# Performance work log

Measured on AMD Instinct MI355X. Metric: run time of the kernel, lower is better.

Reference implementation:

```python
import jax, jax.numpy as jnp
import numpy as np

B, D, H = 2048, 32, 512  # batch, state dim (x has D+1 cols incl. logdet slot), MLP hidden


def setup_inputs() -> dict:
    key = jax.random.key(0)
    ks = jax.random.split(key, 6)
    return {
        "t": jax.random.uniform(ks[0], (1,), dtype=jnp.float32),
        "x": jax.random.normal(ks[1], (B, D + 1), dtype=jnp.float32),
        "W1": jax.random.normal(ks[2], (D + 1, H), dtype=jnp.float32) / np.float32(np.sqrt(D + 1)),
        "b1": jnp.zeros((H,), jnp.float32),
        "W2": jax.random.normal(ks[3], (H, H), dtype=jnp.float32) / np.float32(np.sqrt(H)),
        "b2": jnp.zeros((H,), jnp.float32),
        "W3": jax.random.normal(ks[4], (H, D), dtype=jnp.float32) / np.float32(np.sqrt(H)),
        "b3": jnp.zeros((D,), jnp.float32),
    }


def _vf_single(xi, t, W1, b1, W2, b2, W3, b3):
    # single-sample vector field: R^D -> R^D, time t concatenated as a feature
    inp = jnp.concatenate([xi, t])  # (D+1,)
    h = jnp.tanh(inp @ W1 + b1)
    h = jnp.tanh(h @ W2 + b2)
    return h @ W3 + b3


def reference(t, x, W1, b1, W2, b2, W3, b3):
    xs = x[..., :-1]  # (B, D): drop logdet accumulator column
    # batched vector field dx = vf(t, xs)
    tt = jnp.broadcast_to(t, (xs.shape[0], 1))
    inp = jnp.concatenate([xs, tt], axis=-1)  # (B, D+1)
    h = jnp.tanh(inp @ W1 + b1)
    h = jnp.tanh(h @ W2 + b2)
    dx = h @ W3 + b3  # (B, D)
    # exact divergence: trace of per-sample Jacobian (torch vmap(jacrev) equivalent)
    f = lambda xi: _vf_single(xi, t, W1, b1, W2, b2, W3, b3)
    div = jax.vmap(lambda xi: jnp.trace(jax.jacfwd(f)(xi)))(xs)  # (B,)
    return jnp.concatenate([dx, div[:, None]], axis=-1)  # (B, D+1)
```

## Files before the change

### kernel.cpp

```cpp
#include <hip/hip_runtime.h>
#include <math.h>

constexpr int NB = 2048;
constexpr int ND = 32;
constexpr int NH = 512;
constexpr int NKI = NH / 32;

typedef __bf16 bf16x8 __attribute__((ext_vector_type(8)));
typedef __bf16 bf16x4 __attribute__((ext_vector_type(4)));
typedef float floatx4 __attribute__((ext_vector_type(4)));

__device__ inline float fast_tanh(float x) {
  float e = __expf(2.f * x);
  return 1.f - 2.f / (e + 1.f);
}


__global__ __launch_bounds__(256) void k_pre(
    const float* __restrict__ W1, const float* __restrict__ W2,
    const float* __restrict__ W3, __bf16* __restrict__ W2p,
    __bf16* __restrict__ Mp, float* __restrict__ W3T,
    float* __restrict__ out) {
  int g = blockIdx.x * 256 + threadIdx.x;
  for (int idx = g; idx < NB * (ND + 1); idx += 65536) out[idx] = 0.f;
  if (g < ND * NH)
    W3T[g] = W3[(g & (NH - 1)) * ND + (g >> 9)];

  bool doM = blockIdx.x >= 128;
  int gid = (blockIdx.x & 127) * 256 + threadIdx.x;
  int lane = gid & 63;
  int ki = (gid >> 6) & (NKI - 1);
  int ct = gid >> 10;
  int n = ct * 16 + (lane & 15);
  int k0 = ki * 32 + (lane >> 4) * 8;
  long off = (long)gid * 8;

  if (!doM) {
    __bf16 v[8];
#pragma unroll
    for (int j = 0; j < 8; ++j) v[j] = (__bf16)W2[(k0 + j) * NH + n];
    *(bf16x8*)(W2p + off) = *(bf16x8*)v;
  } else {
    float acc[8];
#pragma unroll
    for (int j = 0; j < 8; ++j) acc[j] = 0.f;
    for (int i = 0; i < ND; ++i) {
      float w3 = W3[n * ND + i];
      float4 u = *(const float4*)&W1[i * NH + k0];
      float4 v = *(const float4*)&W1[i * NH + k0 + 4];
      acc[0] += w3 * u.x; acc[1] += w3 * u.y;
      acc[2] += w3 * u.z; acc[3] += w3 * u.w;
      acc[4] += w3 * v.x; acc[5] += w3 * v.y;
      acc[6] += w3 * v.z; acc[7] += w3 * v.w;
    }
    __bf16 v[8];
#pragma unroll
    for (int j = 0; j < 8; ++j)
      v[j] = (__bf16)(W2[(k0 + j) * NH + n] * acc[j]);
    *(bf16x8*)(Mp + off) = *(bf16x8*)v;
  }
}

__global__ __launch_bounds__(256) void k_main(
    const float* __restrict__ x, const float* __restrict__ t,
    const float* __restrict__ W1, const float* __restrict__ b1,
    const __bf16* __restrict__ W2p, const __bf16* __restrict__ Mp,
    const float* __restrict__ b2, const float* __restrict__ W3T,
    const float* __restrict__ b3, float* __restrict__ out) {
  __shared__ __bf16 aH[16 * NH];
  __shared__ __bf16 aD[16 * NH];
  __shared__ float xs[16][36];
  __shared__ float h2s[16][260];
  __shared__ float divred[4][16];

  int bid = blockIdx.x;
  int rt = bid >> 1;
  int half = bid & 1;
  int tid = threadIdx.x;

  for (int idx = tid; idx < 16 * 33; idx += 256) {
    int r = idx / 33, i = idx - r * 33;
    xs[r][i] = x[(rt * 16 + r) * (ND + 1) + i];
  }
  float tv = t[0];
  __syncthreads();

  {
    int r = tid >> 4;
    int cb = (tid & 15) * 4;
#pragma unroll
    for (int it = 0; it < 8; ++it) {
      int c0 = cb + it * 64;
      float4 bb = *(const float4*)&b1[c0];
      float a0 = bb.x, a1 = bb.y, a2 = bb.z, a3 = bb.w;
#pragma unroll
      for (int i = 0; i < ND; ++i) {
        float xv = xs[r][i];
        float4 w = *(const float4*)&W1[i * NH + c0];
        a0 += xv * w.x; a1 += xv * w.y; a2 += xv * w.z; a3 += xv * w.w;
      }
      {
        float4 w = *(const float4*)&W1[ND * NH + c0];
        a0 += tv * w.x; a1 += tv * w.y; a2 += tv * w.z; a3 += tv * w.w;
      }
      float h0 = fast_tanh(a0), h1 = fast_tanh(a1);
      float h2 = fast_tanh(a2), h3 = fast_tanh(a3);
      __bf16 hv[4] = {(__bf16)h0, (__bf16)h1, (__bf16)h2, (__bf16)h3};
      __bf16 dv[4] = {(__bf16)(1.f - h0 * h0), (__bf16)(1.f - h1 * h1),
                      (__bf16)(1.f - h2 * h2), (__bf16)(1.f - h3 * h3)};
      int ki = c0 >> 5;
      int lane = r | (((c0 >> 3) & 3) << 4);
      int j = c0 & 7;
      int ofs = (ki * 64 + lane) * 8 + j;
      *(bf16x4*)(aH + ofs) = *(bf16x4*)hv;
      *(bf16x4*)(aD + ofs) = *(bf16x4*)dv;
    }
  }
  __syncthreads();

  int w = tid >> 6, lane = tid & 63;
  int col = lane & 15, quad = lane >> 4;
  int ct0 = half * 16 + w * 4;

  floatx4 accH[4] = {{0,0,0,0},{0,0,0,0},{0,0,0,0},{0,0,0,0}};
  floatx4 accM[4] = {{0,0,0,0},{0,0,0,0},{0,0,0,0},{0,0,0,0}};
#pragma unroll 2
  for (int ki = 0; ki < NKI; ++ki) {
    bf16x8 ah = *(const bf16x8*)(aH + (ki * 64 + lane) * 8);
    bf16x8 ad = *(const bf16x8*)(aD + (ki * 64 + lane) * 8);
#pragma unroll
    for (int c = 0; c < 4; ++c) {
      long boff = ((long)((ct0 + c) * NKI + ki) * 64 + lane) * 8;
      bf16x8 bw = *(const bf16x8*)(W2p + boff);
      bf16x8 bm = *(const bf16x8*)(Mp + boff);
      accH[c] = __builtin_amdgcn_mfma_f32_16x16x32_bf16(ah, bw, accH[c], 0, 0, 0);
      accM[c] = __builtin_amdgcn_mfma_f32_16x16x32_bf16(ad, bm, accM[c], 0, 0, 0);
    }
  }

  float divv[4] = {0.f, 0.f, 0.f, 0.f};
#pragma unroll
  for (int c = 0; c < 4; ++c) {
    int n = (ct0 + c) * 16 + col;
    int nc = (w * 4 + c) * 16 + col;
    float bb = b2[n];
#pragma unroll
    for (int r = 0; r < 4; ++r) {
      float h2 = fast_tanh(accH[c][r] + bb);
      h2s[quad * 4 + r][nc] = h2;
      divv[r] += accM[c][r] * (1.f - h2 * h2);
    }
  }
#pragma unroll
  for (int r = 0; r < 4; ++r) {
    float v = divv[r];
    v += __shfl_xor(v, 1);
    v += __shfl_xor(v, 2);
    v += __shfl_xor(v, 4);
    v += __shfl_xor(v, 8);
    if (col == 0) divred[w][quad * 4 + r] = v;
  }
  __syncthreads();
  if (tid < 16) {
    float v = divred[0][tid] + divred[1][tid] + divred[2][tid] + divred[3][tid];
    atomicAdd(&out[(rt * 16 + tid) * (ND + 1) + ND], v);
  }

  int row = tid & 15;
  int i0 = tid >> 4;
  const float* w3a = W3T + (long)(i0 * 2 + 0) * NH + half * 256;
  const float* w3b = W3T + (long)(i0 * 2 + 1) * NH + half * 256;
  float a0 = 0.f, a1 = 0.f;
#pragma unroll 4
  for (int kk = 0; kk < 256; kk += 4) {
    float4 h = *(const float4*)&h2s[row][kk];
    float4 wa = *(const float4*)&w3a[kk];
    float4 wb = *(const float4*)&w3b[kk];
    a0 += h.x * wa.x + h.y * wa.y + h.z * wa.z + h.w * wa.w;
    a1 += h.x * wb.x + h.y * wb.y + h.z * wb.z + h.w * wb.w;
  }
  if (half == 0) { a0 += b3[i0 * 2]; a1 += b3[i0 * 2 + 1]; }
  float* orow = out + (long)(rt * 16 + row) * (ND + 1);
  atomicAdd(&orow[i0 * 2], a0);
  atomicAdd(&orow[i0 * 2 + 1], a1);
}

extern "C" void kernel_launch(void* const* d_in, const int* in_sizes, int n_in,
                              void* d_out, int out_size, void* d_ws, size_t ws_size,
                              hipStream_t stream) {
  const float* t  = (const float*)d_in[0];
  const float* x  = (const float*)d_in[1];
  const float* W1 = (const float*)d_in[2];
  const float* b1 = (const float*)d_in[3];
  const float* W2 = (const float*)d_in[4];
  const float* b2 = (const float*)d_in[5];
  const float* W3 = (const float*)d_in[6];
  const float* b3 = (const float*)d_in[7];
  float* out = (float*)d_out;

  __bf16* W2p = (__bf16*)d_ws;
  __bf16* Mp  = W2p + NH * NH;
  float*  W3T = (float*)(Mp + NH * NH);

  k_pre<<<256, 256, 0, stream>>>(W1, W2, W3, W2p, Mp, W3T, out);
  k_main<<<256, 256, 0, stream>>>(x, t, W1, b1, W2p, Mp, b2, W3T, b3, out);
}
```

Before: 104.7 us.

## Compute first layer with MFMA and retile main kernel to 32 rows by quarter columns

Moves the first-layer matmul (x concatenated with t, times W1) from scalar FMAs onto bf16 MFMA, using a packed W1 prepared in the pre-kernel. The main kernel now handles 32 rows by a quarter of the hidden columns per block instead of 16 rows by a half, so each W2/M fragment is reused across two row tiles. This is meant to cut redundant first-layer work and global weight traffic per output. The cost is that each block recomputes the full first layer for its 32 rows across four column-quarter blocks, and W1 and x are now rounded to bf16.

```diff
diff --git a/kernel.cpp b/kernel.cpp
--- a/kernel.cpp
+++ b/kernel.cpp
@@ -7,7 +7,6 @@
 constexpr int NKI = NH / 32;
 
 typedef __bf16 bf16x8 __attribute__((ext_vector_type(8)));
-typedef __bf16 bf16x4 __attribute__((ext_vector_type(4)));
 typedef float floatx4 __attribute__((ext_vector_type(4)));
 
 __device__ inline float fast_tanh(float x) {
@@ -20,11 +19,25 @@
     const float* __restrict__ W1, const float* __restrict__ W2,
     const float* __restrict__ W3, __bf16* __restrict__ W2p,
     __bf16* __restrict__ Mp, float* __restrict__ W3T,
-    float* __restrict__ out) {
+    __bf16* __restrict__ W1p, float* __restrict__ out) {
   int g = blockIdx.x * 256 + threadIdx.x;
   for (int idx = g; idx < NB * (ND + 1); idx += 65536) out[idx] = 0.f;
   if (g < ND * NH)
     W3T[g] = W3[(g & (NH - 1)) * ND + (g >> 9)];
+  if (g < 4096) {
+    int lane1 = g & 63;
+    int ki1 = (g >> 6) & 1;
+    int ct1 = g >> 7;
+    int n1 = ct1 * 16 + (lane1 & 15);
+    int k0 = ki1 * 32 + (lane1 >> 4) * 8;
+    __bf16 v[8];
+#pragma unroll
+    for (int j = 0; j < 8; ++j) {
+      int k = k0 + j;
+      v[j] = (k <= ND) ? (__bf16)W1[k * NH + n1] : (__bf16)0.f;
+    }
+    *(bf16x8*)(W1p + (long)g * 8) = *(bf16x8*)v;
+  }
 
   bool doM = blockIdx.x >= 128;
   int gid = (blockIdx.x & 127) * 256 + threadIdx.x;
@@ -63,126 +76,150 @@
 
 __global__ __launch_bounds__(256) void k_main(
     const float* __restrict__ x, const float* __restrict__ t,
-    const float* __restrict__ W1, const float* __restrict__ b1,
+    const __bf16* __restrict__ W1p, const float* __restrict__ b1,
     const __bf16* __restrict__ W2p, const __bf16* __restrict__ Mp,
     const float* __restrict__ b2, const float* __restrict__ W3T,
     const float* __restrict__ b3, float* __restrict__ out) {
-  __shared__ __bf16 aH[16 * NH];
-  __shared__ __bf16 aD[16 * NH];
-  __shared__ float xs[16][36];
-  __shared__ float h2s[16][260];
-  __shared__ float divred[4][16];
+  __shared__ __bf16 xf[2 * 2 * 64 * 8];
+  __shared__ __bf16 aH[2 * 16 * 64 * 8];
+  __shared__ __bf16 aD[2 * 16 * 64 * 8];
+  __shared__ float h2s[32][132];
+  __shared__ float divred[4][32];
 
   int bid = blockIdx.x;
-  int rt = bid >> 1;
-  int half = bid & 1;
+  int rb = bid >> 2;
+  int q = bid & 3;
   int tid = threadIdx.x;
-
-  for (int idx = tid; idx < 16 * 33; idx += 256) {
-    int r = idx / 33, i = idx - r * 33;
-    xs[r][i] = x[(rt * 16 + r) * (ND + 1) + i];
-  }
-  float tv = t[0];
-  __syncthreads();
-
-  {
-    int r = tid >> 4;
-    int cb = (tid & 15) * 4;
-#pragma unroll
-    for (int it = 0; it < 8; ++it) {
-      int c0 = cb + it * 64;
-      float4 bb = *(const float4*)&b1[c0];
-      float a0 = bb.x, a1 = bb.y, a2 = bb.z, a3 = bb.w;
-#pragma unroll
-      for (int i = 0; i < ND; ++i) {
-        float xv = xs[r][i];
-        float4 w = *(const float4*)&W1[i * NH + c0];
-        a0 += xv * w.x; a1 += xv * w.y; a2 += xv * w.z; a3 += xv * w.w;
-      }
-      {
-        float4 w = *(const float4*)&W1[ND * NH + c0];
-        a0 += tv * w.x; a1 += tv * w.y; a2 += tv * w.z; a3 += tv * w.w;
-      }
-      float h0 = fast_tanh(a0), h1 = fast_tanh(a1);
-      float h2 = fast_tanh(a2), h3 = fast_tanh(a3);
-      __bf16 hv[4] = {(__bf16)h0, (__bf16)h1, (__bf16)h2, (__bf16)h3};
-      __bf16 dv[4] = {(__bf16)(1.f - h0 * h0), (__bf16)(1.f - h1 * h1),
-                      (__bf16)(1.f - h2 * h2), (__bf16)(1.f - h3 * h3)};
-      int ki = c0 >> 5;
-      int lane = r | (((c0 >> 3) & 3) << 4);
-      int j = c0 & 7;
-      int ofs = (ki * 64 + lane) * 8 + j;
-      *(bf16x4*)(aH + ofs) = *(bf16x4*)hv;
-      *(bf16x4*)(aD + ofs) = *(bf16x4*)dv;
-    }
-  }
-  __syncthreads();
-
   int w = tid >> 6, lane = tid & 63;
   int col = lane & 15, quad = lane >> 4;
-  int ct0 = half * 16 + w * 4;
-
-  floatx4 accH[4] = {{0,0,0,0},{0,0,0,0},{0,0,0,0},{0,0,0,0}};
-  floatx4 accM[4] = {{0,0,0,0},{0,0,0,0},{0,0,0,0},{0,0,0,0}};
+  float tv = t[0];
+
+  {
+    int lane0 = tid & 63;
+    int ki0 = (tid >> 6) & 1;
+    int rt0 = tid >> 7;
+    int row = rb * 32 + rt0 * 16 + (lane0 & 15);
+    int k0 = ki0 * 32 + (lane0 >> 4) * 8;
+    __bf16 v[8];
+#pragma unroll
+    for (int j = 0; j < 8; ++j) {
+      int k = k0 + j;
+      float val = (k < ND) ? x[(long)row * (ND + 1) + k] : (k == ND ? tv : 0.f);
+      v[j] = (__bf16)val;
+    }
+    *(bf16x8*)(xf + (long)tid * 8) = *(bf16x8*)v;
+  }
+  __syncthreads();
+
+  {
+    bf16x8 xa[2][2];
+#pragma unroll
+    for (int rt = 0; rt < 2; ++rt)
+#pragma unroll
+      for (int ki = 0; ki < 2; ++ki)
+        xa[rt][ki] = *(const bf16x8*)(xf + ((rt * 2 + ki) * 64 + lane) * 8);
+#pragma unroll 2
+    for (int c8 = 0; c8 < 8; ++c8) {
+      int ct1 = w * 8 + c8;
+      floatx4 ac0 = {0, 0, 0, 0}, ac1 = {0, 0, 0, 0};
+#pragma unroll
+      for (int ki = 0; ki < 2; ++ki) {
+        bf16x8 bw = *(const bf16x8*)(W1p + ((long)(ct1 * 2 + ki) * 64 + lane) * 8);
+        ac0 = __builtin_amdgcn_mfma_f32_16x16x32_bf16(xa[0][ki], bw, ac0, 0, 0, 0);
+        ac1 = __builtin_amdgcn_mfma_f32_16x16x32_bf16(xa[1][ki], bw, ac1, 0, 0, 0);
+      }
+      int n = ct1 * 16 + col;
+      float bb = b1[n];
+      int kio = n >> 5, hi = (n >> 3) & 3, j = n & 7;
+#pragma unroll
+      for (int rt = 0; rt < 2; ++rt) {
+        floatx4 a = rt ? ac1 : ac0;
+#pragma unroll
+        for (int r = 0; r < 4; ++r) {
+          float h = fast_tanh(a[r] + bb);
+          int lanep = (quad * 4 + r) | (hi << 4);
+          int ofs = ((rt * 16 + kio) * 64 + lanep) * 8 + j;
+          aH[ofs] = (__bf16)h;
+          aD[ofs] = (__bf16)(1.f - h * h);
+        }
+      }
+    }
+  }
+  __syncthreads();
+
+  int ct0 = q * 8 + w * 2;
+  floatx4 accH[2][2] = {{{0,0,0,0},{0,0,0,0}},{{0,0,0,0},{0,0,0,0}}};
+  floatx4 accM[2][2] = {{{0,0,0,0},{0,0,0,0}},{{0,0,0,0},{0,0,0,0}}};
 #pragma unroll 2
   for (int ki = 0; ki < NKI; ++ki) {
-    bf16x8 ah = *(const bf16x8*)(aH + (ki * 64 + lane) * 8);
-    bf16x8 ad = *(const bf16x8*)(aD + (ki * 64 + lane) * 8);
-#pragma unroll
-    for (int c = 0; c < 4; ++c) {
-      long boff = ((long)((ct0 + c) * NKI + ki) * 64 + lane) * 8;
+    bf16x8 ah0 = *(const bf16x8*)(aH + ((0 * 16 + ki) * 64 + lane) * 8);
+    bf16x8 ah1 = *(const bf16x8*)(aH + ((1 * 16 + ki) * 64 + lane) * 8);
+    bf16x8 ad0 = *(const bf16x8*)(aD + ((0 * 16 + ki) * 64 + lane) * 8);
+    bf16x8 ad1 = *(const bf16x8*)(aD + ((1 * 16 + ki) * 64 + lane) * 8);
+#pragma unroll
+    for (int cc = 0; cc < 2; ++cc) {
+      long boff = ((long)((ct0 + cc) * NKI + ki) * 64 + lane) * 8;
       bf16x8 bw = *(const bf16x8*)(W2p + boff);
       bf16x8 bm = *(const bf16x8*)(Mp + boff);
-      accH[c] = __builtin_amdgcn_mfma_f32_16x16x32_bf16(ah, bw, accH[c], 0, 0, 0);
-      accM[c] = __builtin_amdgcn_mfma_f32_16x16x32_bf16(ad, bm, accM[c], 0, 0, 0);
-    }
-  }
-
-  float divv[4] = {0.f, 0.f, 0.f, 0.f};
-#pragma unroll
-  for (int c = 0; c < 4; ++c) {
-    int n = (ct0 + c) * 16 + col;
-    int nc = (w * 4 + c) * 16 + col;
+      accH[0][cc] = __builtin_amdgcn_mfma_f32_16x16x32_bf16(ah0, bw, accH[0][cc], 0, 0, 0);
+      accH[1][cc] = __builtin_amdgcn_mfma_f32_16x16x32_bf16(ah1, bw, accH[1][cc], 0, 0, 0);
+      accM[0][cc] = __builtin_amdgcn_mfma_f32_16x16x32_bf16(ad0, bm, accM[0][cc], 0, 0, 0);
+      accM[1][cc] = __builtin_amdgcn_mfma_f32_16x16x32_bf16(ad1, bm, accM[1][cc], 0, 0, 0);
+    }
+  }
+
+  float divv[2][4] = {{0, 0, 0, 0}, {0, 0, 0, 0}};
+#pragma unroll
+  for (int cc = 0; cc < 2; ++cc) {
+    int n = (ct0 + cc) * 16 + col;
+    int nc = (w * 2 + cc) * 16 + col;
     float bb = b2[n];
 #pragma unroll
+    for (int rt = 0; rt < 2; ++rt) {
+#pragma unroll
+      for (int r = 0; r < 4; ++r) {
+        float h2 = fast_tanh(accH[rt][cc][r] + bb);
+        h2s[rt * 16 + quad * 4 + r][nc] = h2;
+        divv[rt][r] += accM[rt][cc][r] * (1.f - h2 * h2);
+      }
+    }
+  }
+#pragma unroll
+  for (int rt = 0; rt < 2; ++rt) {
+#pragma unroll
     for (int r = 0; r < 4; ++r) {
-      float h2 = fast_tanh(accH[c][r] + bb);
-      h2s[quad * 4 + r][nc] = h2;
-      divv[r] += accM[c][r] * (1.f - h2 * h2);
-    }
-  }
-#pragma unroll
-  for (int r = 0; r < 4; ++r) {
-    float v = divv[r];
-    v += __shfl_xor(v, 1);
-    v += __shfl_xor(v, 2);
-    v += __shfl_xor(v, 4);
-    v += __shfl_xor(v, 8);
-    if (col == 0) divred[w][quad * 4 + r] = v;
+      float v = divv[rt][r];
+      v += __shfl_xor(v, 1);
+      v += __shfl_xor(v, 2);
+      v += __shfl_xor(v, 4);
+      v += __shfl_xor(v, 8);
+      if (col == 0) divred[w][rt * 16 + quad * 4 + r] = v;
+    }
   }
   __syncthreads();
-  if (tid < 16) {
+  if (tid < 32) {
     float v = divred[0][tid] + divred[1][tid] + divred[2][tid] + divred[3][tid];
-    atomicAdd(&out[(rt * 16 + tid) * (ND + 1) + ND], v);
-  }
-
-  int row = tid & 15;
-  int i0 = tid >> 4;
-  const float* w3a = W3T + (long)(i0 * 2 + 0) * NH + half * 256;
-  const float* w3b = W3T + (long)(i0 * 2 + 1) * NH + half * 256;
-  float a0 = 0.f, a1 = 0.f;
-#pragma unroll 4
-  for (int kk = 0; kk < 256; kk += 4) {
+    atomicAdd(&out[(long)(rb * 32 + tid) * (ND + 1) + ND], v);
+  }
+
+  int row = tid & 31;
+  int i0 = tid >> 5;
+  float a4[4] = {0.f, 0.f, 0.f, 0.f};
+#pragma unroll 2
+  for (int kk = 0; kk < 128; kk += 4) {
     float4 h = *(const float4*)&h2s[row][kk];
-    float4 wa = *(const float4*)&w3a[kk];
-    float4 wb = *(const float4*)&w3b[kk];
-    a0 += h.x * wa.x + h.y * wa.y + h.z * wa.z + h.w * wa.w;
-    a1 += h.x * wb.x + h.y * wb.y + h.z * wb.z + h.w * wb.w;
-  }
-  if (half == 0) { a0 += b3[i0 * 2]; a1 += b3[i0 * 2 + 1]; }
-  float* orow = out + (long)(rt * 16 + row) * (ND + 1);
-  atomicAdd(&orow[i0 * 2], a0);
-  atomicAdd(&orow[i0 * 2 + 1], a1);
+#pragma unroll
+    for (int ii = 0; ii < 4; ++ii) {
+      float4 wv = *(const float4*)&W3T[(long)(i0 * 4 + ii) * NH + q * 128 + kk];
+      a4[ii] += h.x * wv.x + h.y * wv.y + h.z * wv.z + h.w * wv.w;
+    }
+  }
+  float* orow = out + (long)(rb * 32 + row) * (ND + 1);
+#pragma unroll
+  for (int ii = 0; ii < 4; ++ii) {
+    float v = a4[ii] + (q == 0 ? b3[i0 * 4 + ii] : 0.f);
+    atomicAdd(&orow[i0 * 4 + ii], v);
+  }
 }
 
 extern "C" void kernel_launch(void* const* d_in, const int* in_sizes, int n_in,
@@ -201,7 +238,8 @@
   __bf16* W2p = (__bf16*)d_ws;
   __bf16* Mp  = W2p + NH * NH;
   float*  W3T = (float*)(Mp + NH * NH);
-
-  k_pre<<<256, 256, 0, stream>>>(W1, W2, W3, W2p, Mp, W3T, out);
-  k_main<<<256, 256, 0, stream>>>(x, t, W1, b1, W2p, Mp, b2, W3T, b3, out);
-}
+  __bf16* W1p = (__bf16*)(W3T + ND * NH);
+
+  k_pre<<<256, 256, 0, stream>>>(W1, W2, W3, W2p, Mp, W3T, W1p, out);
+  k_main<<<256, 256, 0, stream>>>(x, t, W1p, b1, W2p, Mp, b2, W3T, b3, out);
+}
```

Result: no change. 103.0 us (-1.6%).
